# Performance work log

Hardware: AMD Instinct MI355X
Metric: run time of the kernel (lower is better)

## Reference

```python
import jax, jax.numpy as jnp
import numpy as np

NUM_GROUPS = 32
EPS = 1e-5
HEAD_DIM = 64

def group_norm(x, w, b):
    # x: [B,C,H,W]; normalize within 32 groups over (C//32, H, W)
    B, C, H, W = x.shape
    xg = x.reshape(B, NUM_GROUPS, C // NUM_GROUPS, H, W)
    mu = xg.mean(axis=(2, 3, 4), keepdims=True)
    var = xg.var(axis=(2, 3, 4), keepdims=True)
    xn = ((xg - mu) / jnp.sqrt(var + EPS)).reshape(B, C, H, W)
    return xn * w[None, :, None, None] + b[None, :, None, None]

def conv1x1(x, w, b):
    # w: [Cout, Cin], b: [Cout]
    return jnp.einsum('bchw,oc->bohw', x, w) + b[None, :, None, None]

def setup_inputs() -> dict:
    key = jax.random.key(0)
    ks = jax.random.split(key, 12)
    B, C, Cc, H, W = 16, 512, 512, 32, 32
    s = 0.02
    return {
        'x': jax.random.normal(ks[0], (B, C, H, W), jnp.float32),
        'context': jax.random.normal(ks[1], (B, Cc, H, W), jnp.float32),
        'norm_q_w': jnp.ones((C,), jnp.float32),
        'norm_q_b': jnp.zeros((C,), jnp.float32),
        'norm_kv_w': jnp.ones((Cc,), jnp.float32),
        'norm_kv_b': jnp.zeros((Cc,), jnp.float32),
        'conv_q_w': jax.random.normal(ks[2], (C, C), jnp.float32) * s,
        'conv_q_b': jnp.zeros((C,), jnp.float32),
        'conv_kv_w': jax.random.normal(ks[3], (2 * C, Cc), jnp.float32) * s,
        'conv_kv_b': jnp.zeros((2 * C,), jnp.float32),
        'proj_w': jax.random.normal(ks[4], (C, C), jnp.float32) * s,
        'proj_b': jnp.zeros((C,), jnp.float32),
    }

def reference(x, context, norm_q_w, norm_q_b, norm_kv_w, norm_kv_b,
              conv_q_w, conv_q_b, conv_kv_w, conv_kv_b, proj_w, proj_b):
    B, C, H, W = x.shape
    nh = max(1, C // HEAD_DIM)
    hd = C // nh
    q = conv1x1(group_norm(x, norm_q_w, norm_q_b), conv_q_w, conv_q_b)
    kv = conv1x1(group_norm(context, norm_kv_w, norm_kv_b), conv_kv_w, conv_kv_b)
    k, v = jnp.split(kv, 2, axis=1)
    L = H * W
    q = q.reshape(B, nh, hd, L)
    k = k.reshape(B, nh, hd, L)
    v = v.reshape(B, nh, hd, L)
    attn = jnp.einsum('bhdi,bhdj->bhij', q, k) * (hd ** -0.5)
    attn = jax.nn.softmax(attn, axis=-1)
    out = jnp.einsum('bhij,bhdj->bhdi', attn, v)
    return x + conv1x1(out.reshape(B, C, H, W), proj_w, proj_b)
```

## Files before the change

kernel.cpp:

```cpp
#include <hip/hip_runtime.h>
#include <hip/hip_bf16.h>

typedef short v8s __attribute__((ext_vector_type(8)));
typedef float v4f __attribute__((ext_vector_type(4)));
typedef float v16f __attribute__((ext_vector_type(16)));
typedef __hip_bfloat16 bf16;

__device__ __forceinline__ float b2f(bf16 h) { return __bfloat162float(h); }
__device__ __forceinline__ bf16 f2b(float f) { return __float2bfloat16(f); }

#define QSCALE 0.18033688f

__device__ __forceinline__ void gll16(const void* g, void* l) {
    __builtin_amdgcn_global_load_lds(
        (const __attribute__((address_space(1))) void*)g,
        (__attribute__((address_space(3))) void*)l, 16, 0, 0);
}

__device__ __forceinline__ unsigned cvtpk(float lo, float hi_) {
    unsigned r;
    asm("v_cvt_pk_bf16_f32 %0, %1, %2" : "=v"(r) : "v"(lo), "v"(hi_));
    return r;
}

__device__ __forceinline__ void pl32swap(unsigned& a, unsigned& b) {
    asm("v_permlane32_swap_b32 %0, %1" : "+v"(a), "+v"(b));
}

__global__ __launch_bounds__(256) void gn_t_kernel(
    const float* __restrict__ x, const float* __restrict__ ctx,
    const float* __restrict__ qw, const float* __restrict__ qb,
    const float* __restrict__ kw, const float* __restrict__ kb,
    bf16* __restrict__ xnT, bf16* __restrict__ cnT)
{
    const int b = blockIdx.y, g = blockIdx.x, z = blockIdx.z, c0 = g * 16;
    const float* src = z ? ctx : x;
    const float* gw  = z ? kw : qw;
    const float* gb  = z ? kb : qb;
    bf16* dst = z ? cnT : xnT;
    __shared__ __attribute__((aligned(16))) bf16 lx[16][1032];
    __shared__ float rS[4], rQ[4];
    __shared__ float sSc[16], sSh[16];
    const int t = threadIdx.x, wave = t >> 6, lane = t & 63;
    const float* xb = src + ((long)b * 512 + c0) * 1024;
    float sum = 0.f, sq = 0.f;
#pragma unroll
    for (int i = 0; i < 16; i++) {
        int q = t + i * 256;
        int ci = q >> 8, l0 = (q & 255) * 4;
        float4 v = *(const float4*)(xb + (long)ci * 1024 + l0);
        sum += v.x + v.y + v.z + v.w;
        sq  += v.x * v.x + v.y * v.y + v.z * v.z + v.w * v.w;
        union { short4 s4v; bf16 h[4]; } w;
        w.h[0] = f2b(v.x); w.h[1] = f2b(v.y); w.h[2] = f2b(v.z); w.h[3] = f2b(v.w);
        *(short4*)&lx[ci][l0] = w.s4v;
    }
#pragma unroll
    for (int off = 32; off > 0; off >>= 1) {
        sum += __shfl_down(sum, off);
        sq  += __shfl_down(sq, off);
    }
    if (lane == 0) { rS[wave] = sum; rQ[wave] = sq; }
    __syncthreads();
    if (t < 16) {
        float S = rS[0] + rS[1] + rS[2] + rS[3];
        float Q = rQ[0] + rQ[1] + rQ[2] + rQ[3];
        const float inv_n = 1.f / 16384.f;
        float mean = S * inv_n;
        float var  = Q * inv_n - mean * mean;
        float rstd = rsqrtf(var + 1e-5f);
        float w = gw[c0 + t];
        sSc[t] = rstd * w;
        sSh[t] = gb[c0 + t] - mean * rstd * w;
    }
    __syncthreads();
    {
        const int hf = t & 1, lg = t >> 1;
        const int ch0 = hf * 8, l0 = lg * 8;
        v8s rd[8];
#pragma unroll
        for (int r = 0; r < 8; r++)
            rd[r] = *(const v8s*)&lx[ch0 + r][l0];
        float sc[8], sh[8];
#pragma unroll
        for (int r = 0; r < 8; r++) { sc[r] = sSc[ch0 + r]; sh[r] = sSh[ch0 + r]; }
#pragma unroll
        for (int j = 0; j < 8; j++) {
            union { float4 f4; bf16 h[8]; } o_;
#pragma unroll
            for (int r = 0; r < 8; r++) {
                union { short s; bf16 h; } cv; cv.s = rd[r][j];
                o_.h[r] = f2b(b2f(cv.h) * sc[r] + sh[r]);
            }
            *(float4*)(dst + ((long)b * 1024 + l0 + j) * 512 + c0 + ch0) = o_.f4;
        }
    }
}

__global__ __launch_bounds__(256) void wconv_kernel(
    const float* __restrict__ a, const float* __restrict__ bsrc,
    const float* __restrict__ csrc, bf16* __restrict__ oa,
    bf16* __restrict__ ob, bf16* __restrict__ oc)
{
    int id = blockIdx.x * 256 + threadIdx.x;
    const float* src; bf16* dst; int off;
    if (id < 65536)       { src = a;    dst = oa; off = id; }
    else if (id < 196608) { src = bsrc; dst = ob; off = id - 65536; }
    else                  { src = csrc; dst = oc; off = id - 196608; }
    float4 v = ((const float4*)src)[off];
    union { short4 s4v; bf16 h[4]; } w;
    w.h[0] = f2b(v.x); w.h[1] = f2b(v.y); w.h[2] = f2b(v.z); w.h[3] = f2b(v.w);
    ((short4*)dst)[off] = w.s4v;
}

__global__ __launch_bounds__(256) void qkv_gemm_kernel(
    const bf16* __restrict__ xnT, const bf16* __restrict__ cnT,
    const bf16* __restrict__ wQ, const bf16* __restrict__ wKV,
    bf16* __restrict__ QT, bf16* __restrict__ KT, bf16* __restrict__ Vo,
    const float* __restrict__ cqb, const float* __restrict__ ckvb)
{
    const long PB = 512L * 1024;
    const int blk = blockIdx.x;
    const int xcd = blk & 7, idx = blk >> 3;
    const int half = idx / 96, rr = idx % 96;
    const int op = rr >> 5, bx = rr & 31;
    const int bz = xcd + 8 * half;
    const bf16* A; const bf16* B; bf16* C; const float* bias;
    int nBlkN, N, biasPerM; float scale;
    if (op == 0) {
        A = xnT + bz * PB; B = wQ;  C = QT + bz * PB; bias = cqb;
        nBlkN = 4; N = 512; biasPerM = 0; scale = QSCALE;
    } else if (op == 1) {
        A = cnT + bz * PB; B = wKV; C = KT + bz * PB; bias = ckvb;
        nBlkN = 4; N = 512; biasPerM = 0; scale = 1.0f;
    } else {
        A = wKV + 512L * 512; B = cnT + bz * PB; C = Vo + bz * PB; bias = ckvb + 512;
        nBlkN = 8; N = 1024; biasPerM = 1; scale = 1.0f;
    }
    const int m0 = (bx / nBlkN) * 128, n0 = (bx % nBlkN) * 128;
    __shared__ __attribute__((aligned(16))) char sm[49152];
    bf16 (*lA)[128][32] = (bf16(*)[128][32])sm;
    bf16 (*lB)[128][32] = (bf16(*)[128][32])(sm + 24576);
    const int t = threadIdx.x, wave = t >> 6, lane = t & 63;
    const int quad = lane >> 4, c = lane & 15;
    const int wm = (wave >> 1) * 64, wn = (wave & 1) * 64;
    const int r16 = lane >> 2;
    const int c4 = lane & 3;
    const int cswz = c4 ^ (r16 & 3) ^ ((r16 >> 2) & 1);
    const bf16* Ag[2]; const bf16* Bg[2];
#pragma unroll
    for (int j = 0; j < 2; j++) {
        int seg = wave * 2 + j;
        Ag[j] = A + (long)(m0 + seg * 16 + r16) * 512 + cswz * 8;
        Bg[j] = B + (long)(n0 + seg * 16 + r16) * 512 + cswz * 8;
    }
    auto issue = [&](int k0, int bi) {
#pragma unroll
        for (int j = 0; j < 2; j++) {
            gll16(Ag[j] + k0, &lA[bi][(wave * 2 + j) * 16][0]);
            gll16(Bg[j] + k0, &lB[bi][(wave * 2 + j) * 16][0]);
        }
    };
    v4f acc[4][4] = {};
    issue(0, 0);
    issue(32, 1);
    const int rdsw = (quad ^ (c & 3) ^ ((c >> 2) & 1)) * 8;
    for (int kc = 0; kc < 16; kc++) {
        const int cur = kc % 3;
        asm volatile("s_waitcnt vmcnt(4)" ::: "memory");
        __builtin_amdgcn_s_barrier();
        __builtin_amdgcn_sched_barrier(0);
        issue(((kc + 2) & 15) * 32, (kc + 2) % 3);
        v8s af[4], bfr[4];
#pragma unroll
        for (int mt = 0; mt < 4; mt++)
            af[mt] = *(const v8s*)&lA[cur][wm + mt * 16 + c][rdsw];
#pragma unroll
        for (int nt = 0; nt < 4; nt++)
            bfr[nt] = *(const v8s*)&lB[cur][wn + nt * 16 + c][rdsw];
#pragma unroll
        for (int mt = 0; mt < 4; mt++)
#pragma unroll
            for (int nt = 0; nt < 4; nt++)
                acc[mt][nt] = __builtin_amdgcn_mfma_f32_16x16x32_bf16(
                    af[mt], bfr[nt], acc[mt][nt], 0, 0, 0);
    }
    asm volatile("s_waitcnt vmcnt(0)" ::: "memory");
    __syncthreads();
    bf16 (*lC)[136] = (bf16(*)[136])sm;
#pragma unroll
    for (int mt = 0; mt < 4; mt++) {
#pragma unroll
        for (int nt = 0; nt < 4; nt++) {
#pragma unroll
            for (int r = 0; r < 4; r++) {
                int row = wm + mt * 16 + quad * 4 + r;
                int col = wn + nt * 16 + c;
                float v = (acc[mt][nt][r]
                           + (biasPerM ? bias[m0 + row] : bias[n0 + col])) * scale;
                lC[row][col] = f2b(v);
            }
        }
    }
    __syncthreads();
#pragma unroll
    for (int i = 0; i < 8; i++) {
        int id = t + i * 256;
        int row = id >> 4, ch = id & 15;
        float4 v4 = *(const float4*)&lC[row][ch * 8];
        *(float4*)(C + (long)(m0 + row) * N + n0 + ch * 8) = v4;
    }
}

__global__ __launch_bounds__(256) void gemm_proj_kernel(
    const bf16* __restrict__ A,
    const bf16* __restrict__ B, long sBb,
    float* __restrict__ C,
    const float* __restrict__ bias,
    const float* __restrict__ resid,
    int M, int N)
{
    const int blk = blockIdx.x;
    const int xcd = blk & 7, idx = blk >> 3;
    const int bz = xcd + 8 * (idx & 1);
    const int tile = idx >> 1;
    const int m0 = (tile >> 3) * 128, n0 = (tile & 7) * 128;
    const bf16* Bb = B + (long)bz * sBb;
    __shared__ __attribute__((aligned(16))) char sm[65536];
    bf16 (*lA)[128][64] = (bf16(*)[128][64])sm;
    bf16 (*lB)[128][64] = (bf16(*)[128][64])(sm + 32768);
    const int t = threadIdx.x, wave = t >> 6, lane = t & 63;
    const int quad = lane >> 4, c = lane & 15;
    const int wm = (wave >> 1) * 64, wn = (wave & 1) * 64;
    const int rIS = lane >> 3, chG = (lane & 7) ^ rIS;
    const bf16* Ag[4]; const bf16* Bg[4]; int segr[4];
#pragma unroll
    for (int j = 0; j < 4; j++) {
        int seg = wave + j * 4;
        segr[j] = seg * 8;
        Ag[j] = A + (long)(m0 + segr[j] + rIS) * 512 + chG * 8;
        Bg[j] = Bb + (long)(n0 + segr[j] + rIS) * 512 + chG * 8;
    }
    auto issue = [&](int k0, int bi) {
#pragma unroll
        for (int j = 0; j < 4; j++) {
            gll16(Ag[j] + k0, &lA[bi][segr[j]][0]);
            gll16(Bg[j] + k0, &lB[bi][segr[j]][0]);
        }
    };
    v4f acc[4][4] = {};
    issue(0, 0);
    for (int kc = 0; kc < 8; kc++) {
        const int cur = kc & 1;
        asm volatile("s_waitcnt vmcnt(0)" ::: "memory");
        __builtin_amdgcn_s_barrier();
        __builtin_amdgcn_sched_barrier(0);
        if (kc < 7) issue((kc + 1) * 64, cur ^ 1);
#pragma unroll
        for (int kk = 0; kk < 2; kk++) {
            v8s af[4], bfr[4];
#pragma unroll
            for (int mt = 0; mt < 4; mt++)
                af[mt] = *(const v8s*)&lA[cur][wm + mt * 16 + c][((kk * 4 + quad) ^ (c & 7)) * 8];
#pragma unroll
            for (int nt = 0; nt < 4; nt++)
                bfr[nt] = *(const v8s*)&lB[cur][wn + nt * 16 + c][((kk * 4 + quad) ^ (c & 7)) * 8];
#pragma unroll
            for (int mt = 0; mt < 4; mt++)
#pragma unroll
                for (int nt = 0; nt < 4; nt++)
                    acc[mt][nt] = __builtin_amdgcn_mfma_f32_16x16x32_bf16(
                        af[mt], bfr[nt], acc[mt][nt], 0, 0, 0);
        }
    }
    __syncthreads();
    float (*lC)[128] = (float(*)[128])sm;
#pragma unroll
    for (int mt = 0; mt < 4; mt++) {
#pragma unroll
        for (int nt = 0; nt < 4; nt++) {
#pragma unroll
            for (int r = 0; r < 4; r++) {
                int row = wm + mt * 16 + quad * 4 + r;
                int col = wn + nt * 16 + c;
                lC[row][col] = acc[mt][nt][r] + bias[m0 + row];
            }
        }
    }
    __syncthreads();
    const long base = (long)bz * ((long)M * N);
#pragma unroll
    for (int i = 0; i < 16; i++) {
        int id = t + i * 256;
        int row = id >> 5, ch = id & 31;
        const long goff = base + (long)(m0 + row) * N + n0 + ch * 4;
        float4 v = *(const float4*)&lC[row][ch * 4];
        float4 rr4 = *(const float4*)(resid + goff);
        v.x += rr4.x; v.y += rr4.y; v.z += rr4.z; v.w += rr4.w;
        *(float4*)(C + goff) = v;
    }
}

__global__ __launch_bounds__(256, 2) void attn_kernel(
    const bf16* QT, const bf16* __restrict__ KT,
    const bf16* __restrict__ V, bf16* AOT)
{
    const int nblk = blockIdx.x;
    const int s = nblk >> 3;
    const int it = s & 3;
    const int g = ((s >> 2) << 3) | (nblk & 7);
    const int h = g & 7, b = g >> 3;
    const int i0 = it * 256;
    __shared__ __attribute__((aligned(16))) bf16 lk[3][64][64];
    __shared__ __attribute__((aligned(16))) bf16 lv[3][64][64];
    const int t = threadIdx.x, wave = t >> 6, lane = t & 63;
    const int m31 = lane & 31, hi = lane >> 5;
    const int rIS = lane >> 3, chG = (lane & 7) ^ rIS;
    v8s qf[2][4];
#pragma unroll
    for (int iq = 0; iq < 2; iq++) {
        const bf16* Qb = QT + ((long)b * 1024 + i0 + wave * 64 + iq * 32 + m31) * 512 + h * 64;
#pragma unroll
        for (int ks = 0; ks < 4; ks++)
            qf[iq][ks] = *(const v8s*)(Qb + ks * 16 + hi * 8);
    }
    const bf16* Kg[2]; const bf16* Vg[2];
#pragma unroll
    for (int j = 0; j < 2; j++) {
        int seg = wave * 2 + j;
        Kg[j] = KT + ((long)b * 1024 + seg * 8 + rIS) * 512 + h * 64 + chG * 8;
        Vg[j] = V + ((long)b * 512 + h * 64 + seg * 8 + rIS) * 1024 + chG * 8;
    }
    auto issue = [&](int jtx, int bi) {
#pragma unroll
        for (int j = 0; j < 2; j++) {
            int seg = wave * 2 + j;
            gll16(Kg[j] + (long)jtx * 64 * 512, &lk[bi][seg * 8][0]);
            gll16(Vg[j] + (long)jtx * 64,      &lv[bi][seg * 8][0]);
        }
    };
    issue(0, 0);
    issue(1, 1);
    float lsum0 = 0.f, lsum1 = 0.f;
    v16f o00 = {}, o01 = {}, o10 = {}, o11 = {};

#define SMPV(sj0, sj1, JB)                                                     \
    {                                                                          \
        unsigned u0[8], u1[8];                                                 \
        _Pragma("unroll")                                                      \
        for (int k2 = 0; k2 < 8; k2++) {                                       \
            float p0l = __builtin_amdgcn_exp2f(sj0[2 * k2]);                   \
            float p0h = __builtin_amdgcn_exp2f(sj0[2 * k2 + 1]);               \
            float p1l = __builtin_amdgcn_exp2f(sj1[2 * k2]);                   \
            float p1h = __builtin_amdgcn_exp2f(sj1[2 * k2 + 1]);               \
            lsum0 += p0l + p0h; lsum1 += p1l + p1h;                            \
            u0[k2] = cvtpk(p0l, p0h); u1[k2] = cvtpk(p1l, p1h);                \
        }                                                                      \
        pl32swap(u0[0], u0[2]); pl32swap(u0[1], u0[3]);                        \
        pl32swap(u0[4], u0[6]); pl32swap(u0[5], u0[7]);                        \
        pl32swap(u1[0], u1[2]); pl32swap(u1[1], u1[3]);                        \
        pl32swap(u1[4], u1[6]); pl32swap(u1[5], u1[7]);                        \
        __builtin_amdgcn_s_setprio(1);                                         \
        _Pragma("unroll")                                                      \
        for (int kk = 0; kk < 2; kk++) {                                       \
            union { unsigned w[4]; v8s v; } pf0, pf1;                          \
            pf0.w[0] = u0[4 * kk + 0]; pf0.w[1] = u0[4 * kk + 1];              \
            pf0.w[2] = u0[4 * kk + 2]; pf0.w[3] = u0[4 * kk + 3];              \
            pf1.w[0] = u1[4 * kk + 0]; pf1.w[1] = u1[4 * kk + 1];              \
            pf1.w[2] = u1[4 * kk + 2]; pf1.w[3] = u1[4 * kk + 3];              \
            const int cc2 = ((JB) * 2 + kk) * 2 + hi;                          \
            v8s vf0 = *(const v8s*)&lv[cur][m31][(cc2 ^ (m31 & 7)) * 8];       \
            o00 = __builtin_amdgcn_mfma_f32_32x32x16_bf16(vf0, pf0.v, o00, 0, 0, 0); \
            o10 = __builtin_amdgcn_mfma_f32_32x32x16_bf16(vf0, pf1.v, o10, 0, 0, 0); \
            v8s vf1 = *(const v8s*)&lv[cur][32 + m31][(cc2 ^ (m31 & 7)) * 8];  \
            o01 = __builtin_amdgcn_mfma_f32_32x32x16_bf16(vf1, pf0.v, o01, 0, 0, 0); \
            o11 = __builtin_amdgcn_mfma_f32_32x32x16_bf16(vf1, pf1.v, o11, 0, 0, 0); \
        }                                                                      \
        __builtin_amdgcn_s_setprio(0);                                         \
    }

    for (int jt = 0; jt < 16; jt++) {
        const int cur = jt % 3;
        asm volatile("s_waitcnt vmcnt(4)" ::: "memory");
        __builtin_amdgcn_s_barrier();
        __builtin_amdgcn_sched_barrier(0);
        issue((jt + 2) & 15, (jt + 2) % 3);
        v16f s00 = {}, s01 = {}, s10 = {}, s11 = {};
        __builtin_amdgcn_s_setprio(1);
#pragma unroll
        for (int ks = 0; ks < 4; ks++) {
            const int chs = ((ks * 2 + hi) ^ (m31 & 7)) * 8;
            v8s kf0 = *(const v8s*)&lk[cur][m31][chs];
            v8s kf1 = *(const v8s*)&lk[cur][32 + m31][chs];
            s00 = __builtin_amdgcn_mfma_f32_32x32x16_bf16(kf0, qf[0][ks], s00, 0, 0, 0);
            s01 = __builtin_amdgcn_mfma_f32_32x32x16_bf16(kf0, qf[1][ks], s01, 0, 0, 0);
            s10 = __builtin_amdgcn_mfma_f32_32x32x16_bf16(kf1, qf[0][ks], s10, 0, 0, 0);
            s11 = __builtin_amdgcn_mfma_f32_32x32x16_bf16(kf1, qf[1][ks], s11, 0, 0, 0);
        }
        __builtin_amdgcn_s_setprio(0);
        SMPV(s00, s01, 0)
        SMPV(s10, s11, 1)
    }
#undef SMPV
    {
        float lt0 = lsum0 + __shfl_xor(lsum0, 32);
        float lt1 = lsum1 + __shfl_xor(lsum1, 32);
        float inv0 = 1.f / lt0, inv1 = 1.f / lt1;
#pragma unroll
        for (int iq = 0; iq < 2; iq++) {
            float inv = iq ? inv1 : inv0;
            const v16f& oa = iq ? o10 : o00;
            const v16f& ob = iq ? o11 : o01;
            bf16* Ob = AOT + ((long)b * 1024 + i0 + wave * 64 + iq * 32 + m31) * 512 + h * 64;
#pragma unroll
            for (int gq = 0; gq < 4; gq++) {
                union { short4 s4v; bf16 hh[4]; } w0, w1;
#pragma unroll
                for (int k = 0; k < 4; k++) {
                    w0.hh[k] = f2b(oa[gq * 4 + k] * inv);
                    w1.hh[k] = f2b(ob[gq * 4 + k] * inv);
                }
                *(short4*)(Ob + gq * 8 + hi * 4)      = w0.s4v;
                *(short4*)(Ob + 32 + gq * 8 + hi * 4) = w1.s4v;
            }
        }
    }
}

extern "C" void kernel_launch(void* const* d_in, const int* in_sizes, int n_in,
                              void* d_out, int out_size, void* d_ws, size_t ws_size,
                              hipStream_t stream)
{
    const float* x    = (const float*)d_in[0];
    const float* ctx  = (const float*)d_in[1];
    const float* nqw  = (const float*)d_in[2];
    const float* nqb  = (const float*)d_in[3];
    const float* nkw  = (const float*)d_in[4];
    const float* nkb  = (const float*)d_in[5];
    const float* cqw  = (const float*)d_in[6];
    const float* cqb  = (const float*)d_in[7];
    const float* ckvw = (const float*)d_in[8];
    const float* ckvb = (const float*)d_in[9];
    const float* pw   = (const float*)d_in[10];
    const float* pb   = (const float*)d_in[11];
    float* out = (float*)d_out;
    bf16* ws  = (bf16*)d_ws;

    const long PB  = 512L * 1024;
    const long TOT = 16L * PB;
    bf16* s0 = ws;
    bf16* s1 = ws + TOT;
    bf16* s2 = ws + 2 * TOT;
    bf16* s3 = ws + 3 * TOT;
    bf16* s4 = ws + 4 * TOT;
    bf16* wQ  = ws + 5 * TOT;
    bf16* wKV = wQ + 262144;
    bf16* wP  = wKV + 524288;

    dim3 blk(256);
    gn_t_kernel<<<dim3(32, 16, 2), blk, 0, stream>>>(
        x, ctx, nqw, nqb, nkw, nkb, s0, s1);
    wconv_kernel<<<dim3(1024), blk, 0, stream>>>(cqw, ckvw, pw, wQ, wKV, wP);
    qkv_gemm_kernel<<<dim3(1536), blk, 0, stream>>>(
        s0, s1, wQ, wKV, s2, s3, s4, cqb, ckvb);
    attn_kernel<<<dim3(512), blk, 0, stream>>>(s2, s3, s4, s2);
    gemm_proj_kernel<<<dim3(512), blk, 0, stream>>>(
        wP, s2, PB, out, pb, x, 512, 1024);
}
```

Measured before the change: 230.7 us.

## Fuse weight conversion into groupnorm launch, triple-buffer proj GEMM, fix LDS swizzles

```diff
diff --git a/kernel.cpp b/kernel.cpp
--- a/kernel.cpp
+++ b/kernel.cpp
@@ -31,9 +31,30 @@
     const float* __restrict__ x, const float* __restrict__ ctx,
     const float* __restrict__ qw, const float* __restrict__ qb,
     const float* __restrict__ kw, const float* __restrict__ kb,
-    bf16* __restrict__ xnT, bf16* __restrict__ cnT)
+    bf16* __restrict__ xnT, bf16* __restrict__ cnT,
+    const float* __restrict__ cqw, const float* __restrict__ ckvw,
+    const float* __restrict__ pw,
+    bf16* __restrict__ wQ, bf16* __restrict__ wKV, bf16* __restrict__ wP)
 {
     const int b = blockIdx.y, g = blockIdx.x, z = blockIdx.z, c0 = g * 16;
+    const int t = threadIdx.x;
+    if (z == 2) {
+        int w = blockIdx.y * 32 + blockIdx.x;
+#pragma unroll
+        for (int i = 0; i < 2; i++) {
+            int id = w * 512 + i * 256 + t;
+            const float* src; bf16* dst; int off;
+            if (id < 65536)       { src = cqw;  dst = wQ;  off = id; }
+            else if (id < 196608) { src = ckvw; dst = wKV; off = id - 65536; }
+            else                  { src = pw;   dst = wP;  off = id - 196608; }
+            float4 v = ((const float4*)src)[off];
+            union { short4 s4v; bf16 h[4]; } wv;
+            wv.h[0] = f2b(v.x); wv.h[1] = f2b(v.y);
+            wv.h[2] = f2b(v.z); wv.h[3] = f2b(v.w);
+            ((short4*)dst)[off] = wv.s4v;
+        }
+        return;
+    }
     const float* src = z ? ctx : x;
     const float* gw  = z ? kw : qw;
     const float* gb  = z ? kb : qb;
@@ -41,7 +62,7 @@
     __shared__ __attribute__((aligned(16))) bf16 lx[16][1032];
     __shared__ float rS[4], rQ[4];
     __shared__ float sSc[16], sSh[16];
-    const int t = threadIdx.x, wave = t >> 6, lane = t & 63;
+    const int wave = t >> 6, lane = t & 63;
     const float* xb = src + ((long)b * 512 + c0) * 1024;
     float sum = 0.f, sq = 0.f;
 #pragma unroll
@@ -95,22 +116,6 @@
             *(float4*)(dst + ((long)b * 1024 + l0 + j) * 512 + c0 + ch0) = o_.f4;
         }
     }
-}
-
-__global__ __launch_bounds__(256) void wconv_kernel(
-    const float* __restrict__ a, const float* __restrict__ bsrc,
-    const float* __restrict__ csrc, bf16* __restrict__ oa,
-    bf16* __restrict__ ob, bf16* __restrict__ oc)
-{
-    int id = blockIdx.x * 256 + threadIdx.x;
-    const float* src; bf16* dst; int off;
-    if (id < 65536)       { src = a;    dst = oa; off = id; }
-    else if (id < 196608) { src = bsrc; dst = ob; off = id - 65536; }
-    else                  { src = csrc; dst = oc; off = id - 196608; }
-    float4 v = ((const float4*)src)[off];
-    union { short4 s4v; bf16 h[4]; } w;
-    w.h[0] = f2b(v.x); w.h[1] = f2b(v.y); w.h[2] = f2b(v.z); w.h[3] = f2b(v.w);
-    ((short4*)dst)[off] = w.s4v;
 }
 
 __global__ __launch_bounds__(256) void qkv_gemm_kernel(
@@ -226,78 +231,82 @@
     const int tile = idx >> 1;
     const int m0 = (tile >> 3) * 128, n0 = (tile & 7) * 128;
     const bf16* Bb = B + (long)bz * sBb;
-    __shared__ __attribute__((aligned(16))) char sm[65536];
-    bf16 (*lA)[128][64] = (bf16(*)[128][64])sm;
-    bf16 (*lB)[128][64] = (bf16(*)[128][64])(sm + 32768);
+    __shared__ __attribute__((aligned(16))) char sm[49152];
+    bf16 (*lA)[128][32] = (bf16(*)[128][32])sm;
+    bf16 (*lB)[128][32] = (bf16(*)[128][32])(sm + 24576);
     const int t = threadIdx.x, wave = t >> 6, lane = t & 63;
     const int quad = lane >> 4, c = lane & 15;
     const int wm = (wave >> 1) * 64, wn = (wave & 1) * 64;
-    const int rIS = lane >> 3, chG = (lane & 7) ^ rIS;
-    const bf16* Ag[4]; const bf16* Bg[4]; int segr[4];
-#pragma unroll
-    for (int j = 0; j < 4; j++) {
-        int seg = wave + j * 4;
-        segr[j] = seg * 8;
-        Ag[j] = A + (long)(m0 + segr[j] + rIS) * 512 + chG * 8;
-        Bg[j] = Bb + (long)(n0 + segr[j] + rIS) * 512 + chG * 8;
+    const int r16 = lane >> 2, c4 = lane & 3;
+    const int cswz = c4 ^ (r16 & 3) ^ ((r16 >> 2) & 1);
+    const bf16* Ag[2]; const bf16* Bg[2];
+#pragma unroll
+    for (int j = 0; j < 2; j++) {
+        int seg = wave * 2 + j;
+        Ag[j] = A + (long)(m0 + seg * 16 + r16) * 512 + cswz * 8;
+        Bg[j] = Bb + (long)(n0 + seg * 16 + r16) * 512 + cswz * 8;
     }
     auto issue = [&](int k0, int bi) {
 #pragma unroll
-        for (int j = 0; j < 4; j++) {
-            gll16(Ag[j] + k0, &lA[bi][segr[j]][0]);
-            gll16(Bg[j] + k0, &lB[bi][segr[j]][0]);
+        for (int j = 0; j < 2; j++) {
+            gll16(Ag[j] + k0, &lA[bi][(wave * 2 + j) * 16][0]);
+            gll16(Bg[j] + k0, &lB[bi][(wave * 2 + j) * 16][0]);
         }
     };
     v4f acc[4][4] = {};
     issue(0, 0);
-    for (int kc = 0; kc < 8; kc++) {
-        const int cur = kc & 1;
-        asm volatile("s_waitcnt vmcnt(0)" ::: "memory");
+    issue(32, 1);
+    const int rdsw = (quad ^ (c & 3) ^ ((c >> 2) & 1)) * 8;
+    for (int kc = 0; kc < 16; kc++) {
+        const int cur = kc % 3;
+        asm volatile("s_waitcnt vmcnt(4)" ::: "memory");
         __builtin_amdgcn_s_barrier();
         __builtin_amdgcn_sched_barrier(0);
-        if (kc < 7) issue((kc + 1) * 64, cur ^ 1);
-#pragma unroll
-        for (int kk = 0; kk < 2; kk++) {
-            v8s af[4], bfr[4];
-#pragma unroll
-            for (int mt = 0; mt < 4; mt++)
-                af[mt] = *(const v8s*)&lA[cur][wm + mt * 16 + c][((kk * 4 + quad) ^ (c & 7)) * 8];
+        issue(((kc + 2) & 15) * 32, (kc + 2) % 3);
+        v8s af[4], bfr[4];
+#pragma unroll
+        for (int mt = 0; mt < 4; mt++)
+            af[mt] = *(const v8s*)&lA[cur][wm + mt * 16 + c][rdsw];
+#pragma unroll
+        for (int nt = 0; nt < 4; nt++)
+            bfr[nt] = *(const v8s*)&lB[cur][wn + nt * 16 + c][rdsw];
+#pragma unroll
+        for (int mt = 0; mt < 4; mt++)
 #pragma unroll
             for (int nt = 0; nt < 4; nt++)
-                bfr[nt] = *(const v8s*)&lB[cur][wn + nt * 16 + c][((kk * 4 + quad) ^ (c & 7)) * 8];
-#pragma unroll
-            for (int mt = 0; mt < 4; mt++)
-#pragma unroll
-                for (int nt = 0; nt < 4; nt++)
-                    acc[mt][nt] = __builtin_amdgcn_mfma_f32_16x16x32_bf16(
-                        af[mt], bfr[nt], acc[mt][nt], 0, 0, 0);
-        }
-    }
+                acc[mt][nt] = __builtin_amdgcn_mfma_f32_16x16x32_bf16(
+                    af[mt], bfr[nt], acc[mt][nt], 0, 0, 0);
+    }
+    asm volatile("s_waitcnt vmcnt(0)" ::: "memory");
     __syncthreads();
     float (*lC)[128] = (float(*)[128])sm;
-#pragma unroll
-    for (int mt = 0; mt < 4; mt++) {
-#pragma unroll
-        for (int nt = 0; nt < 4; nt++) {
-#pragma unroll
-            for (int r = 0; r < 4; r++) {
-                int row = wm + mt * 16 + quad * 4 + r;
-                int col = wn + nt * 16 + c;
-                lC[row][col] = acc[mt][nt][r] + bias[m0 + row];
-            }
-        }
-    }
-    __syncthreads();
     const long base = (long)bz * ((long)M * N);
 #pragma unroll
-    for (int i = 0; i < 16; i++) {
-        int id = t + i * 256;
-        int row = id >> 5, ch = id & 31;
-        const long goff = base + (long)(m0 + row) * N + n0 + ch * 4;
-        float4 v = *(const float4*)&lC[row][ch * 4];
-        float4 rr4 = *(const float4*)(resid + goff);
-        v.x += rr4.x; v.y += rr4.y; v.z += rr4.z; v.w += rr4.w;
-        *(float4*)(C + goff) = v;
+    for (int hh = 0; hh < 2; hh++) {
+        if ((wave >> 1) == hh) {
+#pragma unroll
+            for (int mt = 0; mt < 4; mt++)
+#pragma unroll
+                for (int nt = 0; nt < 4; nt++)
+#pragma unroll
+                    for (int r = 0; r < 4; r++) {
+                        int row = mt * 16 + quad * 4 + r;
+                        int col = wn + nt * 16 + c;
+                        lC[row][col] = acc[mt][nt][r] + bias[m0 + hh * 64 + row];
+                    }
+        }
+        __syncthreads();
+#pragma unroll
+        for (int i = 0; i < 8; i++) {
+            int id = t + i * 256;
+            int row = id >> 5, ch = id & 31;
+            const long goff = base + (long)(m0 + hh * 64 + row) * N + n0 + ch * 4;
+            float4 v = *(const float4*)&lC[row][ch * 4];
+            float4 rr4 = *(const float4*)(resid + goff);
+            v.x += rr4.x; v.y += rr4.y; v.z += rr4.z; v.w += rr4.w;
+            *(float4*)(C + goff) = v;
+        }
+        __syncthreads();
     }
 }
 
@@ -316,6 +325,7 @@
     const int t = threadIdx.x, wave = t >> 6, lane = t & 63;
     const int m31 = lane & 31, hi = lane >> 5;
     const int rIS = lane >> 3, chG = (lane & 7) ^ rIS;
+    const int rb = ((m31 >> 3) & 1) << 2;
     v8s qf[2][4];
 #pragma unroll
     for (int iq = 0; iq < 2; iq++) {
@@ -328,8 +338,9 @@
 #pragma unroll
     for (int j = 0; j < 2; j++) {
         int seg = wave * 2 + j;
-        Kg[j] = KT + ((long)b * 1024 + seg * 8 + rIS) * 512 + h * 64 + chG * 8;
-        Vg[j] = V + ((long)b * 512 + h * 64 + seg * 8 + rIS) * 1024 + chG * 8;
+        int ch2 = (chG ^ (j << 2)) * 8;
+        Kg[j] = KT + ((long)b * 1024 + seg * 8 + rIS) * 512 + h * 64 + ch2;
+        Vg[j] = V + ((long)b * 512 + h * 64 + seg * 8 + rIS) * 1024 + ch2;
     }
     auto issue = [&](int jtx, int bi) {
 #pragma unroll
@@ -369,10 +380,10 @@
             pf1.w[0] = u1[4 * kk + 0]; pf1.w[1] = u1[4 * kk + 1];              \
             pf1.w[2] = u1[4 * kk + 2]; pf1.w[3] = u1[4 * kk + 3];              \
             const int cc2 = ((JB) * 2 + kk) * 2 + hi;                          \
-            v8s vf0 = *(const v8s*)&lv[cur][m31][(cc2 ^ (m31 & 7)) * 8];       \
+            v8s vf0 = *(const v8s*)&lv[cur][m31][(cc2 ^ (m31 & 7) ^ rb) * 8];  \
             o00 = __builtin_amdgcn_mfma_f32_32x32x16_bf16(vf0, pf0.v, o00, 0, 0, 0); \
             o10 = __builtin_amdgcn_mfma_f32_32x32x16_bf16(vf0, pf1.v, o10, 0, 0, 0); \
-            v8s vf1 = *(const v8s*)&lv[cur][32 + m31][(cc2 ^ (m31 & 7)) * 8];  \
+            v8s vf1 = *(const v8s*)&lv[cur][32 + m31][(cc2 ^ (m31 & 7) ^ rb) * 8]; \
             o01 = __builtin_amdgcn_mfma_f32_32x32x16_bf16(vf1, pf0.v, o01, 0, 0, 0); \
             o11 = __builtin_amdgcn_mfma_f32_32x32x16_bf16(vf1, pf1.v, o11, 0, 0, 0); \
         }                                                                      \
@@ -389,7 +400,7 @@
         __builtin_amdgcn_s_setprio(1);
 #pragma unroll
         for (int ks = 0; ks < 4; ks++) {
-            const int chs = ((ks * 2 + hi) ^ (m31 & 7)) * 8;
+            const int chs = ((ks * 2 + hi) ^ (m31 & 7) ^ rb) * 8;
             v8s kf0 = *(const v8s*)&lk[cur][m31][chs];
             v8s kf1 = *(const v8s*)&lk[cur][32 + m31][chs];
             s00 = __builtin_amdgcn_mfma_f32_32x32x16_bf16(kf0, qf[0][ks], s00, 0, 0, 0);
@@ -458,9 +469,8 @@
     bf16* wP  = wKV + 524288;
 
     dim3 blk(256);
-    gn_t_kernel<<<dim3(32, 16, 2), blk, 0, stream>>>(
-        x, ctx, nqw, nqb, nkw, nkb, s0, s1);
-    wconv_kernel<<<dim3(1024), blk, 0, stream>>>(cqw, ckvw, pw, wQ, wKV, wP);
+    gn_t_kernel<<<dim3(32, 16, 3), blk, 0, stream>>>(
+        x, ctx, nqw, nqb, nkw, nkb, s0, s1, cqw, ckvw, pw, wQ, wKV, wP);
     qkv_gemm_kernel<<<dim3(1536), blk, 0, stream>>>(
         s0, s1, wQ, wKV, s2, s3, s4, cqb, ckvb);
     attn_kernel<<<dim3(512), blk, 0, stream>>>(s2, s3, s4, s2);
```

After: 230.9 us. About the same (+0.1%).
